# Performance work log

Measured on AMD Instinct MI355X. Metric: run time of the kernel, lower is better.

## Reference

```python
import jax, jax.numpy as jnp
import numpy as np

T, H, NH, NKV, HD, E, K, I = 1024, 2048, 16, 4, 128, 16, 2, 768
EPS = 1e-6
THETA = 10000.0


def setup_inputs() -> dict:
    key = jax.random.key(0)
    ks = jax.random.split(key, 8)
    s = 0.02
    return {
        "hidden_states": jax.random.normal(ks[0], (T, H), jnp.float32),
        "positions": jnp.arange(T, dtype=jnp.int32),
        "w_norm1": jnp.ones((H,), jnp.float32),
        "w_norm2": jnp.ones((H,), jnp.float32),
        "w_qkv": jax.random.normal(ks[1], (H, (NH + 2 * NKV) * HD), jnp.float32) * s,
        "w_qnorm": jnp.ones((HD,), jnp.float32),
        "w_knorm": jnp.ones((HD,), jnp.float32),
        "w_o": jax.random.normal(ks[2], (NH * HD, H), jnp.float32) * s,
        "w_router": jax.random.normal(ks[3], (H, E), jnp.float32) * s,
        "w_gate": jax.random.normal(ks[4], (E, H, I), jnp.float32) * s,
        "w_up": jax.random.normal(ks[5], (E, H, I), jnp.float32) * s,
        "w_down": jax.random.normal(ks[6], (E, I, H), jnp.float32) * s,
    }


def rmsnorm(x, w):
    return x * jax.lax.rsqrt(jnp.mean(x * x, axis=-1, keepdims=True) + EPS) * w


def apply_rope(x, positions):
    # NEOX-style rotary, full head_dim. x: [T, n_heads, HD]
    half = HD // 2
    inv_freq = 1.0 / (THETA ** (jnp.arange(half, dtype=jnp.float32) / half))
    ang = positions.astype(jnp.float32)[:, None] * inv_freq  # [T, half]
    cos = jnp.cos(ang)[:, None, :]
    sin = jnp.sin(ang)[:, None, :]
    x1, x2 = x[..., :half], x[..., half:]
    return jnp.concatenate([x1 * cos - x2 * sin, x2 * cos + x1 * sin], axis=-1)


def reference(hidden_states, positions, w_norm1, w_norm2, w_qkv, w_qnorm, w_knorm,
              w_o, w_router, w_gate, w_up, w_down):
    # prepare_attn: residual = x; h = input_layernorm(x)
    residual = hidden_states
    h = rmsnorm(hidden_states, w_norm1)

    # --- attention (bidirectional, GQA, per-head q/k RMSNorm + RoPE) ---
    qkv = h @ w_qkv
    q, k, v = jnp.split(qkv, [NH * HD, NH * HD + NKV * HD], axis=-1)
    q = rmsnorm(q.reshape(T, NH, HD), w_qnorm)
    k = rmsnorm(k.reshape(T, NKV, HD), w_knorm)
    v = v.reshape(T, NKV, HD)
    q = apply_rope(q, positions)
    k = apply_rope(k, positions)
    rep = NH // NKV
    kf = jnp.repeat(k, rep, axis=1)  # [T, NH, HD]
    vf = jnp.repeat(v, rep, axis=1)
    scores = jnp.einsum('tnd,snd->nts', q, kf) * (HD ** -0.5)  # [NH, T, T]
    p = jax.nn.softmax(scores, axis=-1)
    ctx = jnp.einsum('nts,snd->tnd', p, vf).reshape(T, NH * HD)
    attn_out = ctx @ w_o

    # prepare_mlp: residual = residual + attn_out; h = post_attention_layernorm(residual)
    residual = residual + attn_out
    h = rmsnorm(residual, w_norm2)

    # --- sparse MoE: softmax router, top-k renormalize, SwiGLU experts ---
    logits = h @ w_router
    probs = jax.nn.softmax(logits, axis=-1)
    topw, topi = jax.lax.top_k(probs, K)
    topw = topw / jnp.sum(topw, axis=-1, keepdims=True)
    gates = jnp.zeros((T, E), h.dtype).at[jnp.arange(T)[:, None], topi].set(topw)
    g = jnp.einsum('th,ehi->eti', h, w_gate)
    u = jnp.einsum('th,ehi->eti', h, w_up)
    y = jnp.einsum('eti,eih->eth', jax.nn.silu(g) * u, w_down)
    moe_out = jnp.einsum('eth,te->th', y, gates)

    return moe_out, residual
```

## Files before the change

kernel.cpp:

```cpp
#include <hip/hip_runtime.h>

#define T_    1024
#define H_    2048
#define NH_   16
#define NKV_  4
#define HD_   128
#define E_    16
#define I_    768
#define QKVN  3072

typedef __attribute__((ext_vector_type(8))) short  short8;
typedef __attribute__((ext_vector_type(4))) float  f32x4;
typedef unsigned short u16;

#define LDPA 32
#define LDPB 40

__device__ inline u16 f2bf(float f) {
  unsigned u = __builtin_bit_cast(unsigned, f);
  return (u16)((u + 0x7fffu + ((u >> 16) & 1u)) >> 16);
}
__device__ inline float bf2f(u16 h) {
  unsigned u = ((unsigned)h) << 16;
  return __builtin_bit_cast(float, u);
}

__device__ inline void gll16(const u16* g, u16* l) {
  __builtin_amdgcn_global_load_lds(
      (const __attribute__((address_space(1))) void*)g,
      (__attribute__((address_space(3))) void*)l, 16, 0, 0);
}

__device__ inline float blk_sum(float v, float* lds) {
#pragma unroll
  for (int o = 32; o; o >>= 1) v += __shfl_down(v, o);
  int w = threadIdx.x >> 6;
  __syncthreads();
  if ((threadIdx.x & 63) == 0) lds[w] = v;
  __syncthreads();
  float s = lds[0];
  int nw = blockDim.x >> 6;
  for (int i = 1; i < nw; ++i) s += lds[i];
  return s;
}


struct F4 { float v[4]; };

__device__ inline void wrS(u16* lds, const F4& r) {
  int n = threadIdx.x & 63, kh = (threadIdx.x >> 6) * 4;
  uint2 w;
  w.x = (unsigned)f2bf(r.v[0]) | ((unsigned)f2bf(r.v[1]) << 16);
  w.y = (unsigned)f2bf(r.v[2]) | ((unsigned)f2bf(r.v[3]) << 16);
  *(uint2*)(lds + n * LDPB + kh) = w;
}

template<int SA, int SB>
__device__ inline void mma2(const u16* As, const u16* Bs, f32x4 acc[2][2]) {
  const int lane = threadIdx.x & 63, wv = threadIdx.x >> 6;
  const int wr = wv >> 1, wc = wv & 1;
  const int kk = (lane >> 4) * 8, rr = lane & 15;
  short8 aF[2], bF[2];
#pragma unroll
  for (int m = 0; m < 2; ++m)
    aF[m] = *(const short8*)(As + (wr * 32 + m * 16 + rr) * SA + kk);
#pragma unroll
  for (int n = 0; n < 2; ++n)
    bF[n] = *(const short8*)(Bs + (wc * 32 + n * 16 + rr) * SB + kk);
#pragma unroll
  for (int m = 0; m < 2; ++m)
#pragma unroll
    for (int n = 0; n < 2; ++n)
      acc[m][n] = __builtin_amdgcn_mfma_f32_16x16x32_bf16(aF[m], bF[n], acc[m][n], 0, 0, 0);
}

#define ZERO_ACC(acc) do { \
  _Pragma("unroll") for (int m_ = 0; m_ < 2; ++m_) \
  _Pragma("unroll") for (int n_ = 0; n_ < 2; ++n_) acc[m_][n_] = (f32x4){0.f,0.f,0.f,0.f}; \
} while (0)

#define EPI_ROW(m, r)  (((threadIdx.x >> 6) >> 1) * 32 + (m)*16 + (((threadIdx.x&63) >> 4) * 4) + (r))
#define EPI_COL(n)     ((((threadIdx.x >> 6) & 1) * 32) + (n)*16 + ((threadIdx.x&63) & 15))

template<int NT, class GA, class LB>
__device__ inline void pipeGF(GA ga, LB lb, u16* A0, u16* B0, u16* A1, u16* B1,
                              f32x4 acc[2][2]) {
  F4 b0, b1;
  ga(A0, 0);
  lb(b0, 0); lb(b1, 1);
  wrS(B0, b0);
  if (NT > 2) lb(b0, 2);
#pragma unroll 1
  for (int kt = 0; kt < NT; kt += 2) {
    __syncthreads();
    ga(A1, kt + 1);
    wrS(B1, b1);
    if (kt + 3 < NT) lb(b1, kt + 3);
    mma2<LDPA, LDPB>(A0, B0, acc);
    __syncthreads();
    if (kt + 2 < NT) { ga(A0, kt + 2); wrS(B0, b0); }
    if (kt + 4 < NT) lb(b0, kt + 4);
    mma2<LDPA, LDPB>(A1, B1, acc);
  }
}


__global__ __launch_bounds__(256) void k_rms1(const float* x, const float* w, u16* out) {
  __shared__ float lds[4];
  int t = blockIdx.x, tid = threadIdx.x;
  float v[8]; float ss = 0.f;
#pragma unroll
  for (int i = 0; i < 8; ++i) { v[i] = x[(size_t)t * H_ + tid + 256 * i]; ss += v[i] * v[i]; }
  ss = blk_sum(ss, lds);
  float inv = rsqrtf(ss * (1.f / H_) + 1e-6f);
#pragma unroll
  for (int i = 0; i < 8; ++i)
    out[(size_t)t * H_ + tid + 256 * i] = f2bf(v[i] * inv * w[tid + 256 * i]);
}

__global__ __launch_bounds__(256) void k_rms2(const float* x, const float* w,
                                              float* outf, u16* outb) {
  __shared__ float lds[4];
  int t = blockIdx.x, tid = threadIdx.x;
  float v[8]; float ss = 0.f;
#pragma unroll
  for (int i = 0; i < 8; ++i) { v[i] = x[(size_t)t * H_ + tid + 256 * i]; ss += v[i] * v[i]; }
  ss = blk_sum(ss, lds);
  float inv = rsqrtf(ss * (1.f / H_) + 1e-6f);
#pragma unroll
  for (int i = 0; i < 8; ++i) {
    float r = v[i] * inv * w[tid + 256 * i];
    outf[(size_t)t * H_ + tid + 256 * i] = r;
    outb[(size_t)t * H_ + tid + 256 * i] = f2bf(r);
  }
}

__global__ __launch_bounds__(512) void k_qkv(const u16* h1, const float* wqkv, float* qkv) {
  __shared__ __align__(16) u16 A0[128 * LDPA], A1[128 * LDPA];
  __shared__ __align__(16) u16 B0[64 * LDPB], B1[64 * LDPB];
  int bn = blockIdx.x, bm = blockIdx.y;
  f32x4 acc[2][2]; ZERO_ACC(acc);
  auto ga = [&](u16* As, int kt) {
    gll16(h1 + (size_t)(bm * 128 + (threadIdx.x >> 2)) * H_ + kt * 32 + (threadIdx.x & 3) * 8,
          As + (threadIdx.x & 448) * 8);
  };
  auto lb = [&](F4& r, int kt) {
    int n = threadIdx.x & 63, kh = (threadIdx.x >> 6) * 4;
    const float* src = wqkv + (size_t)(kt * 32 + kh) * QKVN + bn * 64 + n;
#pragma unroll
    for (int j = 0; j < 4; ++j) r.v[j] = src[(size_t)j * QKVN];
  };
  pipeGF<H_ / 32>(ga, lb, A0, B0, A1, B1, acc);
#pragma unroll
  for (int m = 0; m < 2; ++m)
#pragma unroll
    for (int n = 0; n < 2; ++n) {
      f32x4 a = acc[m][n];
#pragma unroll
      for (int r = 0; r < 4; ++r)
        qkv[(size_t)(bm * 128 + EPI_ROW(m, r)) * QKVN + bn * 64 + EPI_COL(n)] = a[r];
    }
}

__global__ __launch_bounds__(256) void k_qkrope(const float* qkv, const int* pos,
                                                const float* wq, const float* wk,
                                                u16* q, u16* kk, u16* vT) {
  __shared__ float cs[64], sn[64];
  int t = blockIdx.x, tid = threadIdx.x, lane = tid & 63, w = tid >> 6;
  if (tid < 64) {
    float fr = expf(-((float)tid / 64.f) * 9.210340371976184f);
    float ang = (float)pos[t] * fr;
    float s_, c_; sincosf(ang, &s_, &c_);
    cs[tid] = c_; sn[tid] = s_;
  }
  __syncthreads();
  const float* row = qkv + (size_t)t * QKVN;
  for (int h = w; h < NH_; h += 4) {
    float x1 = row[h * 128 + lane], x2 = row[h * 128 + 64 + lane];
    float ss = x1 * x1 + x2 * x2;
#pragma unroll
    for (int o = 32; o; o >>= 1) ss += __shfl_down(ss, o);
    ss = __shfl(ss, 0);
    float inv = rsqrtf(ss * (1.f / HD_) + 1e-6f);
    float n1 = x1 * inv * wq[lane], n2 = x2 * inv * wq[64 + lane];
    float o1 = n1 * cs[lane] - n2 * sn[lane];
    float o2 = n2 * cs[lane] + n1 * sn[lane];
    q[(size_t)t * (NH_ * HD_) + h * 128 + lane] = f2bf(o1);
    q[(size_t)t * (NH_ * HD_) + h * 128 + 64 + lane] = f2bf(o2);
  }
  if (w < NKV_) {
    int h = w;
    float x1 = row[2048 + h * 128 + lane], x2 = row[2048 + h * 128 + 64 + lane];
    float ss = x1 * x1 + x2 * x2;
#pragma unroll
    for (int o = 32; o; o >>= 1) ss += __shfl_down(ss, o);
    ss = __shfl(ss, 0);
    float inv = rsqrtf(ss * (1.f / HD_) + 1e-6f);
    float n1 = x1 * inv * wk[lane], n2 = x2 * inv * wk[64 + lane];
    float o1 = n1 * cs[lane] - n2 * sn[lane];
    float o2 = n2 * cs[lane] + n1 * sn[lane];
    kk[((size_t)h * T_ + t) * HD_ + lane] = f2bf(o1);
    kk[((size_t)h * T_ + t) * HD_ + 64 + lane] = f2bf(o2);
    float v1 = row[2560 + h * 128 + lane], v2 = row[2560 + h * 128 + 64 + lane];
    vT[((size_t)(h * 128 + lane)) * T_ + t] = f2bf(v1);
    vT[((size_t)(h * 128 + 64 + lane)) * T_ + t] = f2bf(v2);
  }
}

__global__ __launch_bounds__(256) void k_fattn(const u16* q, const u16* kb,
                                               const u16* vT, float* opart, float* lpart) {
  __shared__ __align__(16) u16 Ks[64 * 136];
  __shared__ __align__(16) u16 Vs[128 * 72];
  __shared__ __align__(16) u16 Ps[4 * 16 * 72];
  int h = blockIdx.x, qt = blockIdx.y, kvs = blockIdx.z;
  int tid = threadIdx.x, lane = tid & 63, wv = tid >> 6;
  int rr = lane & 15, kk = (lane >> 4) * 8;
  const u16* kbh = kb + (size_t)(h >> 2) * T_ * HD_;
  const u16* vTh = vT + (size_t)(h >> 2) * HD_ * T_;
  int q0 = qt * 64 + wv * 16;
  short8 qf[4];
#pragma unroll
  for (int ks = 0; ks < 4; ++ks)
    qf[ks] = *(const short8*)(q + (size_t)(q0 + rr) * (NH_ * HD_) + h * 128 + ks * 32 + kk);
  f32x4 oacc[8];
#pragma unroll
  for (int i = 0; i < 8; ++i) oacc[i] = (f32x4){0.f, 0.f, 0.f, 0.f};
  float lsum[4] = {0.f, 0.f, 0.f, 0.f};
  const float scale = 0.08838834764831845f;
  u16* Pw = Ps + wv * 16 * 72;
#pragma unroll 1
  for (int kv = kvs * 4; kv < kvs * 4 + 4; ++kv) {
    __syncthreads();
    {
      uint4 kreg[4];
#pragma unroll
      for (int i = 0; i < 4; ++i) {
        int c = tid + 256 * i;
        kreg[i] = *(const uint4*)(kbh + (size_t)(kv * 64 + (c >> 4)) * HD_ + (c & 15) * 8);
      }
#pragma unroll
      for (int i = 0; i < 4; ++i) {
        int c = tid + 256 * i;
        *(uint4*)(Ks + (c >> 4) * 136 + (c & 15) * 8) = kreg[i];
      }
    }
    {
      uint4 vreg[4];
#pragma unroll
      for (int i = 0; i < 4; ++i) {
        int c = tid + 256 * i;
        vreg[i] = *(const uint4*)(vTh + (size_t)(c >> 3) * T_ + kv * 64 + (c & 7) * 8);
      }
#pragma unroll
      for (int i = 0; i < 4; ++i) {
        int c = tid + 256 * i;
        *(uint4*)(Vs + (c >> 3) * 72 + (c & 7) * 8) = vreg[i];
      }
    }
    __syncthreads();
    f32x4 sacc[4];
#pragma unroll
    for (int nf = 0; nf < 4; ++nf) sacc[nf] = (f32x4){0.f, 0.f, 0.f, 0.f};
#pragma unroll
    for (int ks = 0; ks < 4; ++ks)
#pragma unroll
      for (int nf = 0; nf < 4; ++nf) {
        short8 bF = *(const short8*)(Ks + (nf * 16 + rr) * 136 + ks * 32 + kk);
        sacc[nf] = __builtin_amdgcn_mfma_f32_16x16x32_bf16(qf[ks], bF, sacc[nf], 0, 0, 0);
      }
#pragma unroll
    for (int nf = 0; nf < 4; ++nf)
#pragma unroll
      for (int r = 0; r < 4; ++r) {
        float p = __expf(sacc[nf][r] * scale);
        lsum[r] += p;
        Pw[((lane >> 4) * 4 + r) * 72 + nf * 16 + rr] = f2bf(p);
      }
#pragma unroll
    for (int ks2 = 0; ks2 < 2; ++ks2) {
      short8 pa = *(const short8*)(Pw + rr * 72 + ks2 * 32 + kk);
#pragma unroll
      for (int nd = 0; nd < 8; ++nd) {
        short8 bV = *(const short8*)(Vs + (nd * 16 + rr) * 72 + ks2 * 32 + kk);
        oacc[nd] = __builtin_amdgcn_mfma_f32_16x16x32_bf16(pa, bV, oacc[nd], 0, 0, 0);
      }
    }
  }
#pragma unroll
  for (int r = 0; r < 4; ++r) {
#pragma unroll
    for (int o = 1; o < 16; o <<= 1) lsum[r] += __shfl_xor(lsum[r], o);
  }
  if ((lane & 15) == 0) {
#pragma unroll
    for (int r = 0; r < 4; ++r)
      lpart[((size_t)kvs * NH_ + h) * T_ + q0 + (lane >> 4) * 4 + r] = lsum[r];
  }
  float* op = opart + (size_t)kvs * T_ * (NH_ * HD_);
#pragma unroll
  for (int nd = 0; nd < 8; ++nd)
#pragma unroll
    for (int r = 0; r < 4; ++r)
      op[(size_t)(q0 + (lane >> 4) * 4 + r) * (NH_ * HD_) + h * 128 + nd * 16 + rr] =
          oacc[nd][r];
}

__global__ __launch_bounds__(256) void k_attnfin(const float* opart, const float* lpart,
                                                 u16* ctx) {
  int t = blockIdx.x, tid = threadIdx.x;
#pragma unroll
  for (int i = 0; i < 8; ++i) {
    int idx = tid + 256 * i;
    int h = idx >> 7;
    float l = 0.f, o = 0.f;
#pragma unroll
    for (int s = 0; s < 4; ++s) {
      l += lpart[((size_t)s * NH_ + h) * T_ + t];
      o += opart[(size_t)s * T_ * (NH_ * HD_) + (size_t)t * (NH_ * HD_) + idx];
    }
    ctx[(size_t)t * (NH_ * HD_) + idx] = f2bf(o / l);
  }
}

__global__ __launch_bounds__(512) void k_wo(const u16* ctx, const float* wo,
                                            const float* hs, float* resid) {
  __shared__ __align__(16) u16 A0[128 * LDPA], A1[128 * LDPA];
  __shared__ __align__(16) u16 B0[64 * LDPB], B1[64 * LDPB];
  int bn = blockIdx.x, bm = blockIdx.y;
  f32x4 acc[2][2]; ZERO_ACC(acc);
  auto ga = [&](u16* As, int kt) {
    gll16(ctx + (size_t)(bm * 128 + (threadIdx.x >> 2)) * H_ + kt * 32 + (threadIdx.x & 3) * 8,
          As + (threadIdx.x & 448) * 8);
  };
  auto lb = [&](F4& r, int kt) {
    int n = threadIdx.x & 63, kh = (threadIdx.x >> 6) * 4;
    const float* src = wo + (size_t)(kt * 32 + kh) * H_ + bn * 64 + n;
#pragma unroll
    for (int j = 0; j < 4; ++j) r.v[j] = src[(size_t)j * H_];
  };
  pipeGF<H_ / 32>(ga, lb, A0, B0, A1, B1, acc);
#pragma unroll
  for (int m = 0; m < 2; ++m)
#pragma unroll
    for (int n = 0; n < 2; ++n) {
      f32x4 a = acc[m][n];
#pragma unroll
      for (int r = 0; r < 4; ++r) {
        size_t idx = (size_t)(bm * 128 + EPI_ROW(m, r)) * H_ + bn * 64 + EPI_COL(n);
        resid[idx] = a[r] + hs[idx];
      }
    }
}

__global__ __launch_bounds__(256) void k_router(const float* h2f, const float* wr_,
                                                int* topi, float* topw, int* cnt) {
  __shared__ float xs[H_];
  __shared__ float red[4][16];
  __shared__ float lg[16];
  int t = blockIdx.x, tid = threadIdx.x;
#pragma unroll
  for (int i = 0; i < 8; ++i) xs[tid + 256 * i] = h2f[(size_t)t * H_ + tid + 256 * i];
  __syncthreads();
  int e = tid & 15, p = tid >> 4;
  float s = 0.f;
  int b0 = p * 128;
  for (int i = 0; i < 128; ++i) s += xs[b0 + i] * wr_[(size_t)(b0 + i) * E_ + e];
  s += __shfl_down(s, 32);
  s += __shfl_down(s, 16);
  int lane = tid & 63, w = tid >> 6;
  if (lane < 16) red[w][lane] = s;
  __syncthreads();
  if (tid < 16) lg[tid] = red[0][tid] + red[1][tid] + red[2][tid] + red[3][tid];
  __syncthreads();
  if (tid == 0) {
    float l1 = -1e30f; int e1 = 0;
    for (int i = 0; i < E_; ++i) if (lg[i] > l1) { l1 = lg[i]; e1 = i; }
    float l2 = -1e30f; int e2 = 0;
    for (int i = 0; i < E_; ++i) if (i != e1 && lg[i] > l2) { l2 = lg[i]; e2 = i; }
    float d = __expf(l2 - l1);
    float w1 = 1.f / (1.f + d), w2 = d / (1.f + d);
    topi[2 * t] = e1; topi[2 * t + 1] = e2;
    topw[2 * t] = w1; topw[2 * t + 1] = w2;
    atomicAdd(&cnt[e1], 1);
    atomicAdd(&cnt[e2], 1);
  }
}

__global__ void k_scan(const int* cnt, int* basearr) {
  if (threadIdx.x == 0) {
    int b = 0;
    for (int e = 0; e < E_; ++e) { basearr[e] = b; b += cnt[e]; }
    basearr[E_] = b;
  }
}

__global__ __launch_bounds__(256) void k_assign(const int* topi, const float* topw,
                                                const int* basearr, int* posc,
                                                int* tok, float* wslot) {
  int t = blockIdx.x * 256 + threadIdx.x;
  if (t < T_) {
#pragma unroll
    for (int j = 0; j < 2; ++j) {
      int e = topi[2 * t + j];
      int p = atomicAdd(&posc[e], 1);
      int s = basearr[e] + p;
      tok[s] = t;
      wslot[s] = topw[2 * t + j];
    }
  }
}

__global__ __launch_bounds__(512) void k_gateup(const u16* h2b,
                                                const float* wg, const float* wu,
                                                const int* cnt, const int* basearr, const int* tok,
                                                u16* act) {
  __shared__ __align__(16) u16 A0[128 * LDPA], A1[128 * LDPA];
  __shared__ __align__(16) u16 B0[64 * LDPB], B1[64 * LDPB];
  __shared__ int gat_s[128];
  int e = blockIdx.x;
  int c = cnt[e];
  int mt = blockIdx.z;
  if (mt * 128 >= c) return;
  int basee = basearr[e];
  int gmax = c - mt * 128;
  int n0 = blockIdx.y * 32;
  int tid = threadIdx.x;
  if (tid < 128) {
    int r = mt * 128 + tid;
    gat_s[tid] = (r < c) ? tok[basee + r] : tok[basee];
  }
  __syncthreads();
  int grow = gat_s[tid >> 2];
  const float* Bg = wg + (size_t)e * H_ * I_;
  const float* Bu = wu + (size_t)e * H_ * I_;
  f32x4 acc[2][2]; ZERO_ACC(acc);
  auto ga = [&](u16* As, int kt) {
    gll16(h2b + (size_t)grow * H_ + kt * 32 + (tid & 3) * 8, As + (tid & 448) * 8);
  };
  auto lb = [&](F4& r, int kt) {
    int cidx = tid & 63, kh = (tid >> 6) * 4;
    int fn = cidx >> 4;
    const float* base = (fn & 1) ? Bu : Bg;
    int col = n0 + (fn >> 1) * 16 + (cidx & 15);
    const float* src = base + (size_t)(kt * 32 + kh) * I_ + col;
#pragma unroll
    for (int j = 0; j < 4; ++j) r.v[j] = src[(size_t)j * I_];
  };
  pipeGF<H_ / 32>(ga, lb, A0, B0, A1, B1, acc);
  int slot0 = basee + mt * 128;
  int col = n0 + ((tid >> 6) & 1) * 16 + ((tid & 63) & 15);
#pragma unroll
  for (int m = 0; m < 2; ++m) {
#pragma unroll
    for (int r = 0; r < 4; ++r) {
      int row = EPI_ROW(m, r);
      if (row >= gmax) continue;
      float g = acc[m][0][r], u = acc[m][1][r];
      float sg = g / (1.f + __expf(-g));
      act[(size_t)(slot0 + row) * I_ + col] = f2bf(sg * u);
    }
  }
}

__global__ __launch_bounds__(512) void k_down(const u16* act, const float* wd,
                                              const int* cnt, const int* basearr,
                                              const int* tok, const float* wslot,
                                              float* moe) {
  __shared__ __align__(16) u16 A0[128 * LDPA], A1[128 * LDPA];
  __shared__ __align__(16) u16 B0[64 * LDPB], B1[64 * LDPB];
  int e = blockIdx.y;
  int c = cnt[e];
  int mt = blockIdx.z;
  if (mt * 128 >= c) return;
  int basee = basearr[e];
  int gmax = c - mt * 128;
  int slot0 = basee + mt * 128;
  int n0 = blockIdx.x * 64;
  const u16* Ap = act + (size_t)slot0 * I_;
  const float* Bp = wd + (size_t)e * I_ * H_;
  f32x4 acc[2][2]; ZERO_ACC(acc);
  auto ga = [&](u16* As, int kt) {
    gll16(Ap + (size_t)(threadIdx.x >> 2) * I_ + kt * 32 + (threadIdx.x & 3) * 8,
          As + (threadIdx.x & 448) * 8);
  };
  auto lb = [&](F4& r, int kt) {
    int n = threadIdx.x & 63, kh = (threadIdx.x >> 6) * 4;
    const float* src = Bp + (size_t)(kt * 32 + kh) * H_ + n0 + n;
#pragma unroll
    for (int j = 0; j < 4; ++j) r.v[j] = src[(size_t)j * H_];
  };
  pipeGF<I_ / 32>(ga, lb, A0, B0, A1, B1, acc);
#pragma unroll
  for (int m = 0; m < 2; ++m)
#pragma unroll
    for (int n = 0; n < 2; ++n) {
      f32x4 a = acc[m][n];
#pragma unroll
      for (int r = 0; r < 4; ++r) {
        int row = EPI_ROW(m, r);
        if (row >= gmax) continue;
        int col = EPI_COL(n);
        int slot = slot0 + row;
        float wgt = wslot[slot];
        int tk = tok[slot];
        atomicAdd(&moe[(size_t)tk * H_ + n0 + col], a[r] * wgt);
      }
    }
}

extern "C" void kernel_launch(void* const* d_in, const int* in_sizes, int n_in,
                              void* d_out, int out_size, void* d_ws, size_t ws_size,
                              hipStream_t stream) {
  const float* hs    = (const float*)d_in[0];
  const int*   pos   = (const int*)d_in[1];
  const float* wn1   = (const float*)d_in[2];
  const float* wn2   = (const float*)d_in[3];
  const float* wqkv  = (const float*)d_in[4];
  const float* wqn   = (const float*)d_in[5];
  const float* wkn   = (const float*)d_in[6];
  const float* wo    = (const float*)d_in[7];
  const float* wrt   = (const float*)d_in[8];
  const float* wg    = (const float*)d_in[9];
  const float* wu    = (const float*)d_in[10];
  const float* wd    = (const float*)d_in[11];
  float* out = (float*)d_out;
  float* moe_out = out;
  float* resid   = out + (size_t)T_ * H_;

  char* ws = (char*)d_ws;
  size_t off = 0;
  auto alloc = [&](size_t bytes) { size_t r = off; off = (off + bytes + 255) & ~(size_t)255; return r; };
  u16*   h1    = (u16*)  (ws + alloc((size_t)T_ * H_ * 2));
  float* qkv   = (float*)(ws + alloc((size_t)T_ * QKVN * 4));
  u16*   q     = (u16*)  (ws + alloc((size_t)T_ * NH_ * HD_ * 2));
  u16*   kb    = (u16*)  (ws + alloc((size_t)NKV_ * T_ * HD_ * 2));
  u16*   vT    = (u16*)  (ws + alloc((size_t)NKV_ * HD_ * T_ * 2));
  u16*   ctx   = (u16*)  (ws + alloc((size_t)T_ * NH_ * HD_ * 2));
  float* opart = (float*)(ws + alloc((size_t)4 * T_ * NH_ * HD_ * 4));
  float* lpart = (float*)(ws + alloc((size_t)4 * NH_ * T_ * 4));
  float* h2f   = (float*)(ws + alloc((size_t)T_ * H_ * 4));
  u16*   h2b   = (u16*)  (ws + alloc((size_t)T_ * H_ * 2));
  u16*   act   = (u16*)  (ws + alloc((size_t)(2 * T_ + 256) * I_ * 2));
  int*   topi  = (int*)  (ws + alloc((size_t)T_ * 2 * 4));
  float* topw  = (float*)(ws + alloc((size_t)T_ * 2 * 4));
  int*   cnt   = (int*)  (ws + alloc(32 * 4));
  int*   posc  = cnt + 16;
  int*   base  = (int*)  (ws + alloc(32 * 4));
  int*   tok   = (int*)  (ws + alloc((size_t)(2 * T_ + 128) * 4));
  float* wsl   = (float*)(ws + alloc((size_t)(2 * T_ + 128) * 4));
  (void)ws_size; (void)in_sizes; (void)n_in; (void)out_size;

  hipMemsetAsync(moe_out, 0, (size_t)T_ * H_ * 4, stream);
  hipMemsetAsync(cnt, 0, 32 * 4, stream);

  k_rms1<<<T_, 256, 0, stream>>>(hs, wn1, h1);
  k_qkv<<<dim3(QKVN / 64, T_ / 128), 512, 0, stream>>>(h1, wqkv, qkv);
  k_qkrope<<<T_, 256, 0, stream>>>(qkv, pos, wqn, wkn, q, kb, vT);
  k_fattn<<<dim3(NH_, T_ / 64, 4), 256, 0, stream>>>(q, kb, vT, opart, lpart);
  k_attnfin<<<T_, 256, 0, stream>>>(opart, lpart, ctx);
  k_wo<<<dim3(H_ / 64, T_ / 128), 512, 0, stream>>>(ctx, wo, hs, resid);
  k_rms2<<<T_, 256, 0, stream>>>(resid, wn2, h2f, h2b);
  k_router<<<T_, 256, 0, stream>>>(h2f, wrt, topi, topw, cnt);
  k_scan<<<1, 64, 0, stream>>>(cnt, base);
  k_assign<<<4, 256, 0, stream>>>(topi, topw, base, posc, tok, wsl);
  k_gateup<<<dim3(E_, I_ / 32, T_ / 128), 512, 0, stream>>>(h2b, wg, wu, cnt, base, tok, act);
  k_down<<<dim3(H_ / 64, E_, T_ / 128), 512, 0, stream>>>(act, wd, cnt, base, tok, wsl, moe_out);
}
```

Measured before the change: 331.3 us.

## Stream fp32 weights directly to LDS with triple-buffered async pipeline

Replaces the register-staged fp32 weight loads (load to VGPRs, convert to bf16, write to LDS) with direct global-to-LDS async loads of raw fp32 tiles. The weights are converted to bf16 when MFMA fragments are read. The GEMM main loop becomes a three-stage ring buffer synchronised with explicit vmcnt waits and barriers, which is meant to hide load latency and drop the VGPR round trip. In exchange, LDS use per block grows and the fp32 B fragment reads are strided, unpadded scalar LDS accesses that may cause bank conflicts and add conversion work inside the MMA step.

```diff
diff --git a/kernel.cpp b/kernel.cpp
--- a/kernel.cpp
+++ b/kernel.cpp
@@ -13,9 +13,6 @@
 typedef __attribute__((ext_vector_type(4))) float  f32x4;
 typedef unsigned short u16;
 
-#define LDPA 32
-#define LDPB 40
-
 __device__ inline u16 f2bf(float f) {
   unsigned u = __builtin_bit_cast(unsigned, f);
   return (u16)((u + 0x7fffu + ((u >> 16) & 1u)) >> 16);
@@ -30,6 +27,11 @@
       (const __attribute__((address_space(1))) void*)g,
       (__attribute__((address_space(3))) void*)l, 16, 0, 0);
 }
+__device__ inline void gll16f(const float* g, float* l) {
+  __builtin_amdgcn_global_load_lds(
+      (const __attribute__((address_space(1))) void*)g,
+      (__attribute__((address_space(3))) void*)l, 16, 0, 0);
+}
 
 __device__ inline float blk_sum(float v, float* lds) {
 #pragma unroll
@@ -45,28 +47,23 @@
 }
 
 
-struct F4 { float v[4]; };
-
-__device__ inline void wrS(u16* lds, const F4& r) {
-  int n = threadIdx.x & 63, kh = (threadIdx.x >> 6) * 4;
-  uint2 w;
-  w.x = (unsigned)f2bf(r.v[0]) | ((unsigned)f2bf(r.v[1]) << 16);
-  w.y = (unsigned)f2bf(r.v[2]) | ((unsigned)f2bf(r.v[3]) << 16);
-  *(uint2*)(lds + n * LDPB + kh) = w;
-}
-
-template<int SA, int SB>
-__device__ inline void mma2(const u16* As, const u16* Bs, f32x4 acc[2][2]) {
+__device__ inline void mma2F(const u16* As, const float* Bf, f32x4 acc[2][2]) {
   const int lane = threadIdx.x & 63, wv = threadIdx.x >> 6;
   const int wr = wv >> 1, wc = wv & 1;
   const int kk = (lane >> 4) * 8, rr = lane & 15;
   short8 aF[2], bF[2];
 #pragma unroll
   for (int m = 0; m < 2; ++m)
-    aF[m] = *(const short8*)(As + (wr * 32 + m * 16 + rr) * SA + kk);
-#pragma unroll
-  for (int n = 0; n < 2; ++n)
-    bF[n] = *(const short8*)(Bs + (wc * 32 + n * 16 + rr) * SB + kk);
+    aF[m] = *(const short8*)(As + (wr * 32 + m * 16 + rr) * 32 + kk);
+#pragma unroll
+  for (int n = 0; n < 2; ++n) {
+    int c = wc * 32 + n * 16 + rr;
+    short8 b;
+#pragma unroll
+    for (int j = 0; j < 8; ++j)
+      b[j] = (short)f2bf(Bf[(kk + j) * 64 + c]);
+    bF[n] = b;
+  }
 #pragma unroll
   for (int m = 0; m < 2; ++m)
 #pragma unroll
@@ -82,25 +79,28 @@
 #define EPI_ROW(m, r)  (((threadIdx.x >> 6) >> 1) * 32 + (m)*16 + (((threadIdx.x&63) >> 4) * 4) + (r))
 #define EPI_COL(n)     ((((threadIdx.x >> 6) & 1) * 32) + (n)*16 + ((threadIdx.x&63) & 15))
 
-template<int NT, class GA, class LB>
-__device__ inline void pipeGF(GA ga, LB lb, u16* A0, u16* B0, u16* A1, u16* B1,
-                              f32x4 acc[2][2]) {
-  F4 b0, b1;
-  ga(A0, 0);
-  lb(b0, 0); lb(b1, 1);
-  wrS(B0, b0);
-  if (NT > 2) lb(b0, 2);
+template<int NT, class IA, class IB>
+__device__ inline void pipe3(IA ia, IB ib,
+                             u16* A0, u16* A1, u16* A2,
+                             float* B0, float* B1, float* B2,
+                             f32x4 acc[2][2]) {
+  ia(A0, 0); ib(B0, 0);
+  ia(A1, 1); ib(B1, 1);
+  ia(A2, 2); ib(B2, 2);
+  u16 *a0 = A0, *a1 = A1, *a2 = A2;
+  float *b0 = B0, *b1 = B1, *b2 = B2;
 #pragma unroll 1
-  for (int kt = 0; kt < NT; kt += 2) {
-    __syncthreads();
-    ga(A1, kt + 1);
-    wrS(B1, b1);
-    if (kt + 3 < NT) lb(b1, kt + 3);
-    mma2<LDPA, LDPB>(A0, B0, acc);
-    __syncthreads();
-    if (kt + 2 < NT) { ga(A0, kt + 2); wrS(B0, b0); }
-    if (kt + 4 < NT) lb(b0, kt + 4);
-    mma2<LDPA, LDPB>(A1, B1, acc);
+  for (int t = 0; t < NT; ++t) {
+    int rem = NT - 1 - t;
+    if (rem >= 2)      asm volatile("s_waitcnt vmcnt(4)" ::: "memory");
+    else if (rem == 1) asm volatile("s_waitcnt vmcnt(2)" ::: "memory");
+    else               asm volatile("s_waitcnt vmcnt(0)" ::: "memory");
+    __builtin_amdgcn_s_barrier();
+    mma2F(a0, b0, acc);
+    __builtin_amdgcn_s_barrier();
+    if (t + 3 < NT) { ia(a0, t + 3); ib(b0, t + 3); }
+    u16* ta = a0; a0 = a1; a1 = a2; a2 = ta;
+    float* tb = b0; b0 = b1; b1 = b2; b2 = tb;
   }
 }
 
@@ -136,21 +136,19 @@
 }
 
 __global__ __launch_bounds__(512) void k_qkv(const u16* h1, const float* wqkv, float* qkv) {
-  __shared__ __align__(16) u16 A0[128 * LDPA], A1[128 * LDPA];
-  __shared__ __align__(16) u16 B0[64 * LDPB], B1[64 * LDPB];
-  int bn = blockIdx.x, bm = blockIdx.y;
+  __shared__ __align__(16) u16 A0[128 * 32], A1[128 * 32], A2[128 * 32];
+  __shared__ __align__(16) float B0[32 * 64], B1[32 * 64], B2[32 * 64];
+  int bn = blockIdx.x, bm = blockIdx.y, tid = threadIdx.x;
   f32x4 acc[2][2]; ZERO_ACC(acc);
-  auto ga = [&](u16* As, int kt) {
-    gll16(h1 + (size_t)(bm * 128 + (threadIdx.x >> 2)) * H_ + kt * 32 + (threadIdx.x & 3) * 8,
-          As + (threadIdx.x & 448) * 8);
-  };
-  auto lb = [&](F4& r, int kt) {
-    int n = threadIdx.x & 63, kh = (threadIdx.x >> 6) * 4;
-    const float* src = wqkv + (size_t)(kt * 32 + kh) * QKVN + bn * 64 + n;
-#pragma unroll
-    for (int j = 0; j < 4; ++j) r.v[j] = src[(size_t)j * QKVN];
-  };
-  pipeGF<H_ / 32>(ga, lb, A0, B0, A1, B1, acc);
+  auto ia = [&](u16* As, int kt) {
+    gll16(h1 + (size_t)(bm * 128 + (tid >> 2)) * H_ + kt * 32 + (tid & 3) * 8,
+          As + (tid & 448) * 8);
+  };
+  auto ib = [&](float* Bf, int kt) {
+    gll16f(wqkv + (size_t)(kt * 32 + (tid >> 4)) * QKVN + bn * 64 + (tid & 15) * 4,
+           Bf + (tid & 448) * 4);
+  };
+  pipe3<H_ / 32>(ia, ib, A0, A1, A2, B0, B1, B2, acc);
 #pragma unroll
   for (int m = 0; m < 2; ++m)
 #pragma unroll
@@ -324,21 +322,19 @@
 
 __global__ __launch_bounds__(512) void k_wo(const u16* ctx, const float* wo,
                                             const float* hs, float* resid) {
-  __shared__ __align__(16) u16 A0[128 * LDPA], A1[128 * LDPA];
-  __shared__ __align__(16) u16 B0[64 * LDPB], B1[64 * LDPB];
-  int bn = blockIdx.x, bm = blockIdx.y;
+  __shared__ __align__(16) u16 A0[128 * 32], A1[128 * 32], A2[128 * 32];
+  __shared__ __align__(16) float B0[32 * 64], B1[32 * 64], B2[32 * 64];
+  int bn = blockIdx.x, bm = blockIdx.y, tid = threadIdx.x;
   f32x4 acc[2][2]; ZERO_ACC(acc);
-  auto ga = [&](u16* As, int kt) {
-    gll16(ctx + (size_t)(bm * 128 + (threadIdx.x >> 2)) * H_ + kt * 32 + (threadIdx.x & 3) * 8,
-          As + (threadIdx.x & 448) * 8);
-  };
-  auto lb = [&](F4& r, int kt) {
-    int n = threadIdx.x & 63, kh = (threadIdx.x >> 6) * 4;
-    const float* src = wo + (size_t)(kt * 32 + kh) * H_ + bn * 64 + n;
-#pragma unroll
-    for (int j = 0; j < 4; ++j) r.v[j] = src[(size_t)j * H_];
-  };
-  pipeGF<H_ / 32>(ga, lb, A0, B0, A1, B1, acc);
+  auto ia = [&](u16* As, int kt) {
+    gll16(ctx + (size_t)(bm * 128 + (tid >> 2)) * H_ + kt * 32 + (tid & 3) * 8,
+          As + (tid & 448) * 8);
+  };
+  auto ib = [&](float* Bf, int kt) {
+    gll16f(wo + (size_t)(kt * 32 + (tid >> 4)) * H_ + bn * 64 + (tid & 15) * 4,
+           Bf + (tid & 448) * 4);
+  };
+  pipe3<H_ / 32>(ia, ib, A0, A1, A2, B0, B1, B2, acc);
 #pragma unroll
   for (int m = 0; m < 2; ++m)
 #pragma unroll
@@ -414,8 +410,8 @@
                                                 const float* wg, const float* wu,
                                                 const int* cnt, const int* basearr, const int* tok,
                                                 u16* act) {
-  __shared__ __align__(16) u16 A0[128 * LDPA], A1[128 * LDPA];
-  __shared__ __align__(16) u16 B0[64 * LDPB], B1[64 * LDPB];
+  __shared__ __align__(16) u16 A0[128 * 32], A1[128 * 32], A2[128 * 32];
+  __shared__ __align__(16) float B0[32 * 64], B1[32 * 64], B2[32 * 64];
   __shared__ int gat_s[128];
   int e = blockIdx.x;
   int c = cnt[e];
@@ -434,19 +430,17 @@
   const float* Bg = wg + (size_t)e * H_ * I_;
   const float* Bu = wu + (size_t)e * H_ * I_;
   f32x4 acc[2][2]; ZERO_ACC(acc);
-  auto ga = [&](u16* As, int kt) {
+  auto ia = [&](u16* As, int kt) {
     gll16(h2b + (size_t)grow * H_ + kt * 32 + (tid & 3) * 8, As + (tid & 448) * 8);
   };
-  auto lb = [&](F4& r, int kt) {
-    int cidx = tid & 63, kh = (tid >> 6) * 4;
-    int fn = cidx >> 4;
+  auto ib = [&](float* Bf, int kt) {
+    int n4 = (tid & 15) * 4;
+    int fn = n4 >> 4;
     const float* base = (fn & 1) ? Bu : Bg;
-    int col = n0 + (fn >> 1) * 16 + (cidx & 15);
-    const float* src = base + (size_t)(kt * 32 + kh) * I_ + col;
-#pragma unroll
-    for (int j = 0; j < 4; ++j) r.v[j] = src[(size_t)j * I_];
-  };
-  pipeGF<H_ / 32>(ga, lb, A0, B0, A1, B1, acc);
+    int col = n0 + (fn >> 1) * 16 + (n4 & 15);
+    gll16f(base + (size_t)(kt * 32 + (tid >> 4)) * I_ + col, Bf + (tid & 448) * 4);
+  };
+  pipe3<H_ / 32>(ia, ib, A0, A1, A2, B0, B1, B2, acc);
   int slot0 = basee + mt * 128;
   int col = n0 + ((tid >> 6) & 1) * 16 + ((tid & 63) & 15);
 #pragma unroll
@@ -466,8 +460,8 @@
                                               const int* cnt, const int* basearr,
                                               const int* tok, const float* wslot,
                                               float* moe) {
-  __shared__ __align__(16) u16 A0[128 * LDPA], A1[128 * LDPA];
-  __shared__ __align__(16) u16 B0[64 * LDPB], B1[64 * LDPB];
+  __shared__ __align__(16) u16 A0[128 * 32], A1[128 * 32], A2[128 * 32];
+  __shared__ __align__(16) float B0[32 * 64], B1[32 * 64], B2[32 * 64];
   int e = blockIdx.y;
   int c = cnt[e];
   int mt = blockIdx.z;
@@ -476,20 +470,18 @@
   int gmax = c - mt * 128;
   int slot0 = basee + mt * 128;
   int n0 = blockIdx.x * 64;
+  int tid = threadIdx.x;
   const u16* Ap = act + (size_t)slot0 * I_;
   const float* Bp = wd + (size_t)e * I_ * H_;
   f32x4 acc[2][2]; ZERO_ACC(acc);
-  auto ga = [&](u16* As, int kt) {
-    gll16(Ap + (size_t)(threadIdx.x >> 2) * I_ + kt * 32 + (threadIdx.x & 3) * 8,
-          As + (threadIdx.x & 448) * 8);
-  };
-  auto lb = [&](F4& r, int kt) {
-    int n = threadIdx.x & 63, kh = (threadIdx.x >> 6) * 4;
-    const float* src = Bp + (size_t)(kt * 32 + kh) * H_ + n0 + n;
-#pragma unroll
-    for (int j = 0; j < 4; ++j) r.v[j] = src[(size_t)j * H_];
-  };
-  pipeGF<I_ / 32>(ga, lb, A0, B0, A1, B1, acc);
+  auto ia = [&](u16* As, int kt) {
+    gll16(Ap + (size_t)(tid >> 2) * I_ + kt * 32 + (tid & 3) * 8, As + (tid & 448) * 8);
+  };
+  auto ib = [&](float* Bf, int kt) {
+    gll16f(Bp + (size_t)(kt * 32 + (tid >> 4)) * H_ + n0 + (tid & 15) * 4,
+           Bf + (tid & 448) * 4);
+  };
+  pipe3<I_ / 32>(ia, ib, A0, A1, A2, B0, B1, B2, acc);
 #pragma unroll
   for (int m = 0; m < 2; ++m)
 #pragma unroll
```

Result: slower. 369.0 us (+11.4%).
